# Kernel optimization log

Hardware: AMD Instinct MI355X
Metric: run time of the kernel (lower is better)

The kernel has to match this reference:

```python
import jax, jax.numpy as jnp
import numpy as np

B, L, D_MODEL, N_HEADS = 2, 2048, 2048, 16
HEAD_DIM = D_MODEL // N_HEADS
EPS = 1e-6
ROPE_THETA = 10000.0


def rms_norm(x, scale):
    # normalize over head_dim, learnable per-dim scale (QKNorm)
    var = jnp.mean(jnp.square(x), axis=-1, keepdims=True)
    return x * jax.lax.rsqrt(var + EPS) * scale


def rope(x, offset=0):
    # x: [B, H, T, D]; rotate-half rotary embedding over flattened positions
    T, D = x.shape[-2], x.shape[-1]
    half = D // 2
    inv_freq = 1.0 / (ROPE_THETA ** (jnp.arange(0, half, dtype=jnp.float32) / half))
    pos = jnp.arange(T, dtype=jnp.float32) + offset
    ang = pos[:, None] * inv_freq[None, :]            # [T, half]
    cos, sin = jnp.cos(ang), jnp.sin(ang)
    x1, x2 = x[..., :half], x[..., half:]
    return jnp.concatenate([x1 * cos - x2 * sin, x1 * sin + x2 * cos], axis=-1)


def setup_inputs() -> dict:
    key = jax.random.key(0)
    ks = jax.random.split(key, 7)
    s = 1.0 / np.sqrt(D_MODEL)
    x = jax.random.normal(ks[0], (B, L, D_MODEL), dtype=jnp.float32)
    w_qkv = jax.random.uniform(ks[1], (D_MODEL, 3 * D_MODEL), jnp.float32, -s, s)
    b_qkv = jax.random.uniform(ks[2], (3 * D_MODEL,), jnp.float32, -s, s)
    q_scale = jnp.ones((HEAD_DIM,), jnp.float32)
    k_scale = jnp.ones((HEAD_DIM,), jnp.float32)
    w_out = jax.random.uniform(ks[3], (D_MODEL, D_MODEL), jnp.float32, -s, s)
    b_out = jax.random.uniform(ks[4], (D_MODEL,), jnp.float32, -s, s)
    mask = jnp.tril(jnp.ones((L, L), dtype=bool))   # causal block mask pattern
    return {"x": x, "w_qkv": w_qkv, "b_qkv": b_qkv, "q_scale": q_scale,
            "k_scale": k_scale, "w_out": w_out, "b_out": b_out, "mask": mask}


def reference(x, w_qkv, b_qkv, q_scale, k_scale, w_out, b_out, mask):
    b, t, _ = x.shape
    qkv = x @ w_qkv + b_qkv                                   # [B, T, 3*D]
    qkv = qkv.reshape(b, t, 3, N_HEADS, HEAD_DIM)
    q, k, v = jnp.moveaxis(qkv, 2, 0)                          # each [B, T, H, D]
    q = jnp.transpose(q, (0, 2, 1, 3))                         # [B, H, T, D]
    k = jnp.transpose(k, (0, 2, 1, 3))
    v = jnp.transpose(v, (0, 2, 1, 3))
    q = rms_norm(q, q_scale)
    k = rms_norm(k, k_scale)
    q = rope(q, offset=0)
    k = rope(k, offset=0)
    scores = jnp.einsum('bhqd,bhkd->bhqk', q, k) / np.sqrt(HEAD_DIM)
    scores = jnp.where(mask[None, None, :, :], scores, jnp.float32(-1e30))
    attn = jax.nn.softmax(scores, axis=-1)
    out = jnp.einsum('bhqk,bhkd->bhqd', attn, v)               # [B, H, T, D]
    out = jnp.transpose(out, (0, 2, 1, 3)).reshape(b, t, D_MODEL)
    return out @ w_out + b_out
```

## Files before the change

kernel.cpp:

```cpp
#include <hip/hip_runtime.h>
#include <hip/hip_bf16.h>
#include <stdint.h>


typedef unsigned short ushort8 __attribute__((ext_vector_type(8)));
typedef short          bf16x8 __attribute__((ext_vector_type(8)));
typedef float          f32x4  __attribute__((ext_vector_type(4)));

#define B_   2
#define L_   2048
#define DM   2048
#define NH   16
#define HD   128
#define QKVW 6144

__device__ __forceinline__ uint16_t f2bf(float f){
  uint32_t u = __builtin_bit_cast(uint32_t, f);
  u += 0x7FFFu + ((u >> 16) & 1u);
  return (uint16_t)(u >> 16);
}
__device__ __forceinline__ float bf2f(uint16_t h){
  uint32_t u = ((uint32_t)h) << 16;
  return __builtin_bit_cast(float, u);
}

#define GLD16(gp, lp) __builtin_amdgcn_global_load_lds( \
  (const __attribute__((address_space(1))) void*)(gp),  \
  (__attribute__((address_space(3))) void*)(lp), 16, 0, 0)

__global__ __launch_bounds__(256) void rope_table(float* __restrict__ ct, float* __restrict__ st){
  int i = blockIdx.x * 256 + threadIdx.x;
  int t = i >> 6, d = i & 63;
  float invf = powf(10000.f, -(float)d * (1.f/64.f));
  float s, c;
  sincosf((float)t * invf, &s, &c);
  ct[i] = c; st[i] = s;
}

__global__ __launch_bounds__(256) void cvt_f32_bf16(const float* __restrict__ x,
                                                    uint16_t* __restrict__ o, int n8){
  int i = blockIdx.x * 256 + threadIdx.x;
  if (i < n8){
    const float4* xv = (const float4*)x;
    float4 a = xv[(size_t)i*2], b = xv[(size_t)i*2+1];
    ushort8 v;
    v[0]=f2bf(a.x); v[1]=f2bf(a.y); v[2]=f2bf(a.z); v[3]=f2bf(a.w);
    v[4]=f2bf(b.x); v[5]=f2bf(b.y); v[6]=f2bf(b.z); v[7]=f2bf(b.w);
    *(ushort8*)(o + (size_t)i*8) = v;
  }
}

__global__ __launch_bounds__(256) void transpose_w(const float* __restrict__ W,
                                                   uint16_t* __restrict__ Wt, int R, int C){
  __shared__ float T[64][65];
  const int rb = blockIdx.x, cb = blockIdx.y;
  const int tid = threadIdx.x;
#pragma unroll
  for (int i=0;i<4;i++){
    int rr = i*16 + (tid >> 4);
    int cc = (tid & 15) * 4;
    float4 v = *(const float4*)(W + (size_t)(rb*64 + rr) * C + cb*64 + cc);
    T[rr][cc] = v.x; T[rr][cc+1] = v.y; T[rr][cc+2] = v.z; T[rr][cc+3] = v.w;
  }
  __syncthreads();
  const int oc = tid >> 2, rc = (tid & 3) * 16;
  ushort8 o0, o1;
#pragma unroll
  for (int j=0;j<8;j++){ o0[j] = f2bf(T[rc+j][oc]); o1[j] = f2bf(T[rc+8+j][oc]); }
  size_t ob = (size_t)(cb*64 + oc) * R + rb*64 + rc;
  *(ushort8*)(Wt + ob)     = o0;
  *(ushort8*)(Wt + ob + 8) = o1;
}

template<int MODE>
__global__ __launch_bounds__(512, 2) void gemm8p(
    const uint16_t* __restrict__ A, const uint16_t* __restrict__ Bt,
    const float* __restrict__ bias, void* __restrict__ Cv,
    int M, int N, int K, int nbn,
    const float* __restrict__ qs, const float* __restrict__ ks,
    const float* __restrict__ ct, const float* __restrict__ st)
{
  __shared__ uint16_t LA[3*16384];
  __shared__ uint16_t LB[3*8192];
  __shared__ float sums[4][2][64];
  const int nwg = (M >> 8) * nbn;
  const int q8  = nwg >> 3;
  const int id  = ((int)blockIdx.x & 7) * q8 + ((int)blockIdx.x >> 3);
  const int bm = id / nbn, bn = id % nbn;
  const int tid = threadIdx.x;
  const int lane = tid & 63, w = tid >> 6;
  const int wm = w & 3, wn = w >> 2;
  const int l15 = lane & 15, lh = lane >> 4;
  const int NT = K >> 6;

  const int qs3 = ((lane & 7) ^ ((lane >> 3) & 7)) * 8;
  const uint16_t* gA_ = A  + (size_t)((bm << 8) + (w << 5) + (lane >> 3)) * K + qs3;
  const uint16_t* gB_ = Bt + (size_t)((bn << 7) + (w << 4) + (lane >> 3)) * K + qs3;
  uint16_t* lA_ = LA + (w << 11);
  uint16_t* lB_ = LB + (w << 10);

  const int sw0 = ((lh       ^ (l15 & 7)) << 3);
  const int sw1 = (((4 | lh) ^ (l15 & 7)) << 3);
  const int aoff = (((wm << 6) + l15) << 6);
  const int boff = (((wn << 5) + l15) << 6);
  const int bno[4] = {0, 1024, 4096, 5120};

  f32x4 acc[4][4];
#pragma unroll
  for (int i=0;i<4;i++)
#pragma unroll
    for (int j=0;j<4;j++) acc[i][j] = f32x4{0.f,0.f,0.f,0.f};

  auto STAGE_A = [&](int tt, int s, int i){
    GLD16(gA_ + (size_t)tt*64 + (size_t)(i*8)*K, lA_ + s*16384 + i*512);
  };
  auto STAGE_B = [&](int tt, int s, int i){
    GLD16(gB_ + (size_t)tt*64 + (size_t)(i*8)*K, lB_ + s*8192 + i*512);
  };

#pragma unroll
  for (int i=0;i<4;i++) STAGE_A(0, 0, i);
#pragma unroll
  for (int i=0;i<2;i++) STAGE_B(0, 0, i);
#pragma unroll
  for (int i=0;i<4;i++) STAGE_A(1, 1, i);
#pragma unroll
  for (int i=0;i<2;i++) STAGE_B(1, 1, i);
  asm volatile("s_waitcnt vmcnt(6)" ::: "memory");
  __builtin_amdgcn_s_barrier();

  int sl = 0, sl2 = 2;
  for (int t = 0; t < NT; ++t){
    const bool pf = (t + 2 < NT);
    const uint16_t* la = LA + sl*16384;
    const uint16_t* lb = LB + sl*8192;

    bf16x8 af0[4], bf0[4], af1[4], bf1[4];
#pragma unroll
    for (int mi=0;mi<4;mi++) af0[mi] = *(const bf16x8*)(la + aoff + mi*1024 + sw0);
#pragma unroll
    for (int ni=0;ni<4;ni++) bf0[ni] = *(const bf16x8*)(lb + boff + bno[ni] + sw0);
#pragma unroll
    for (int mi=0;mi<4;mi++) af1[mi] = *(const bf16x8*)(la + aoff + mi*1024 + sw1);
#pragma unroll
    for (int ni=0;ni<4;ni++) bf1[ni] = *(const bf16x8*)(lb + boff + bno[ni] + sw1);
    if (pf){
      STAGE_A(t+2, sl2, 0); STAGE_A(t+2, sl2, 1);
      STAGE_A(t+2, sl2, 2); STAGE_A(t+2, sl2, 3);
      STAGE_B(t+2, sl2, 0); STAGE_B(t+2, sl2, 1);
    }
    __builtin_amdgcn_s_setprio(1);
#pragma unroll
    for (int mi=0;mi<4;mi++)
#pragma unroll
      for (int ni=0;ni<4;ni++)
        acc[mi][ni] = __builtin_amdgcn_mfma_f32_16x16x32_bf16(af0[mi], bf0[ni], acc[mi][ni], 0, 0, 0);
#pragma unroll
    for (int mi=0;mi<4;mi++)
#pragma unroll
      for (int ni=0;ni<4;ni++)
        acc[mi][ni] = __builtin_amdgcn_mfma_f32_16x16x32_bf16(af1[mi], bf1[ni], acc[mi][ni], 0, 0, 0);
    __builtin_amdgcn_s_setprio(0);

    if (t < NT-2)       { asm volatile("s_waitcnt vmcnt(6)" ::: "memory"); }
    else if (t == NT-2) { asm volatile("s_waitcnt vmcnt(0)" ::: "memory"); }
    if (t < NT-1) __builtin_amdgcn_s_barrier();
    sl  = (sl  == 2) ? 0 : sl  + 1;
    sl2 = (sl2 == 2) ? 0 : sl2 + 1;
  }

  const int cm = (bm << 8) + (wm << 6);
  const int cn = (bn << 7);
  int dc[4];
#pragma unroll
  for (int ni=0;ni<4;ni++) dc[ni] = (wn<<5) + ((ni>>1)<<6) + ((ni&1)<<4) + l15;
  float bs[4];
#pragma unroll
  for (int ni=0;ni<4;ni++) bs[ni] = bias[cn + dc[ni]];

  if (MODE == 0){
#pragma unroll
    for (int mi=0;mi<4;mi++)
#pragma unroll
      for (int r=0;r<4;r++){
        int rowg = cm + mi*16 + lh*4 + r;
#pragma unroll
        for (int ni=0;ni<4;ni++)
          ((float*)Cv)[(size_t)rowg * N + cn + dc[ni]] = acc[mi][ni][r] + bs[ni];
      }
  } else {
    uint16_t* Cb = (uint16_t*)Cv;
    const int part = bn >> 4;
    if (part == 2){
#pragma unroll
      for (int mi=0;mi<4;mi++)
#pragma unroll
        for (int r=0;r<4;r++){
          int rowg = cm + mi*16 + lh*4 + r;
#pragma unroll
          for (int ni=0;ni<4;ni++)
            Cb[(size_t)rowg * N + cn + dc[ni]] = f2bf(acc[mi][ni][r] + bs[ni]);
        }
    } else {
      const float* scp = part ? ks : qs;
      float scv[4];
#pragma unroll
      for (int ni=0;ni<4;ni++) scv[ni] = scp[dc[ni]];
      float ssum[4][4];
#pragma unroll
      for (int mi=0;mi<4;mi++)
#pragma unroll
        for (int r=0;r<4;r++){
          float s = 0.f;
#pragma unroll
          for (int ni=0;ni<4;ni++){
            float v = acc[mi][ni][r] + bs[ni];
            acc[mi][ni][r] = v;
            s += v*v;
          }
          s += __shfl_xor(s, 1); s += __shfl_xor(s, 2);
          s += __shfl_xor(s, 4); s += __shfl_xor(s, 8);
          ssum[mi][r] = s;
        }
      if (l15 == 0){
#pragma unroll
        for (int mi=0;mi<4;mi++)
#pragma unroll
          for (int r=0;r<4;r++) sums[wm][wn][mi*16 + lh*4 + r] = ssum[mi][r];
      }
      __syncthreads();
      const int dd0 = (wn<<5) + l15, dd1 = dd0 + 16;
#pragma unroll
      for (int mi=0;mi<4;mi++){
#pragma unroll
        for (int r=0;r<4;r++){
          int rid = mi*16 + lh*4 + r;
          float tot = ssum[mi][r] + sums[wm][wn^1][rid];
          float iv = rsqrtf(tot * 0.0078125f + 1e-6f);
          int rowg = cm + rid;
          int t = rowg & (L_-1);
          float y0 = acc[mi][0][r] * iv * scv[0];
          float y1 = acc[mi][1][r] * iv * scv[1];
          float y2 = acc[mi][2][r] * iv * scv[2];
          float y3 = acc[mi][3][r] * iv * scv[3];
          float c0 = ct[t*64 + dd0], s0 = st[t*64 + dd0];
          float c1 = ct[t*64 + dd1], s1 = st[t*64 + dd1];
          size_t rb_ = (size_t)rowg * N + cn;
          Cb[rb_ + dc[0]] = f2bf(y0*c0 - y2*s0);
          Cb[rb_ + dc[1]] = f2bf(y1*c1 - y3*s1);
          Cb[rb_ + dc[2]] = f2bf(y0*s0 + y2*c0);
          Cb[rb_ + dc[3]] = f2bf(y1*s1 + y3*c1);
        }
      }
    }
  }
}

__global__ __launch_bounds__(256) void transpose_v(const uint16_t* __restrict__ qkv,
                                                   uint16_t* __restrict__ vt){
  __shared__ uint16_t T[64][136];
  const int tb = blockIdx.x, bh = blockIdx.y;
  const int b = bh >> 4, h = bh & 15;
  const int tid = threadIdx.x;
#pragma unroll
  for (int i=0;i<4;i++){
    int g = i*256 + tid, tt = g >> 4, c = g & 15;
    *(ushort8*)(&T[tt][c*8]) =
      *(const ushort8*)(qkv + ((size_t)b*L_ + tb*64 + tt)*QKVW + 2*DM + h*HD + c*8);
  }
  __syncthreads();
  const int d = tid >> 1, th = tid & 1;
#pragma unroll
  for (int i=0;i<4;i++){
    ushort8 o;
#pragma unroll
    for (int j=0;j<8;j++) o[j] = T[th*32 + i*8 + j][d];
    *(ushort8*)(vt + ((size_t)bh*HD + d)*L_ + tb*64 + th*32 + i*8) = o;
  }
}

__global__ __launch_bounds__(256) void flash_attn(
    const uint16_t* __restrict__ qkv, const uint16_t* __restrict__ vt,
    uint16_t* __restrict__ ao)
{
  const int qp = blockIdx.x;
  const int bh = blockIdx.y;
  const int b = bh >> 4, h = bh & 15;
  const int tid = threadIdx.x;
  const int lane = tid & 63, w = tid >> 6;
  const int l15 = lane & 15, lh = lane >> 4;

  __shared__ uint16_t Ks[64][136];
  __shared__ uint16_t Vs[128][72];
  __shared__ uint16_t Ps[4][16][72];

  const float SCL = 0.12751744f;

  for (int sel = 0; sel < 2; sel++){
    const int qb = sel ? (31 - qp) : qp;

    const size_t qrow = (size_t)b * L_ + qb*64 + w*16 + l15;
    const uint16_t* qp_ = qkv + qrow * QKVW + h * HD;
    bf16x8 qf[4];
#pragma unroll
    for (int c = 0; c < 4; c++) qf[c] = *(const bf16x8*)(qp_ + c*32 + lh*8);

    float m_s = -3.0e38f, l_s = 0.f;
    f32x4 oacc[8];
#pragma unroll
    for (int nt = 0; nt < 8; nt++) oacc[nt] = f32x4{0.f,0.f,0.f,0.f};

    const int ntile = qb + 1;
    ushort8 rk[4], rv[4];

#pragma unroll
    for (int i = 0; i < 4; i++){
      int g = i*256 + tid, row = g >> 4, c = g & 15;
      rk[i] = *(const ushort8*)(qkv + ((size_t)b*L_ + row)*QKVW + DM + h*HD + c*8);
    }
#pragma unroll
    for (int i = 0; i < 4; i++){
      int g = i*256 + tid, d = g >> 3, c = g & 7;
      rv[i] = *(const ushort8*)(vt + ((size_t)bh*HD + d)*L_ + c*8);
    }

    for (int kt = 0; kt < ntile; kt++){
      __syncthreads();
#pragma unroll
      for (int i = 0; i < 4; i++){ int g = i*256+tid; *(ushort8*)(&Ks[g>>4][(g&15)*8]) = rk[i]; }
#pragma unroll
      for (int i = 0; i < 4; i++){ int g = i*256+tid; *(ushort8*)(&Vs[g>>3][(g&7)*8]) = rv[i]; }
      __syncthreads();

      if (kt + 1 < ntile){
        const int k2 = (kt + 1) * 64;
#pragma unroll
        for (int i = 0; i < 4; i++){
          int g = i*256 + tid, row = g >> 4, c = g & 15;
          rk[i] = *(const ushort8*)(qkv + ((size_t)b*L_ + k2 + row)*QKVW + DM + h*HD + c*8);
        }
#pragma unroll
        for (int i = 0; i < 4; i++){
          int g = i*256 + tid, d = g >> 3, c = g & 7;
          rv[i] = *(const ushort8*)(vt + ((size_t)bh*HD + d)*L_ + k2 + c*8);
        }
      }

      f32x4 s[4];
#pragma unroll
      for (int nt = 0; nt < 4; nt++) s[nt] = f32x4{0.f,0.f,0.f,0.f};
      __builtin_amdgcn_s_setprio(1);
#pragma unroll
      for (int c = 0; c < 4; c++){
#pragma unroll
        for (int nt = 0; nt < 4; nt++){
          bf16x8 kf = *(const bf16x8*)(&Ks[nt*16 + l15][c*32 + lh*8]);
          s[nt] = __builtin_amdgcn_mfma_f32_16x16x32_bf16(kf, qf[c], s[nt], 0, 0, 0);
        }
      }
      __builtin_amdgcn_s_setprio(0);

      const bool diag = (kt == qb);
      const int qg = w*16 + l15;
      const int kb = lh*4;
#pragma unroll
      for (int nt = 0; nt < 4; nt++){
#pragma unroll
        for (int r = 0; r < 4; r++){
          float v = s[nt][r] * SCL;
          if (diag && (nt*16 + kb + r > qg)) v = -1.0e30f;
          s[nt][r] = v;
        }
      }
      float pm = s[0][0];
#pragma unroll
      for (int nt = 0; nt < 4; nt++)
#pragma unroll
        for (int r = 0; r < 4; r++) pm = fmaxf(pm, s[nt][r]);
      pm = fmaxf(pm, __shfl_xor(pm, 16));
      pm = fmaxf(pm, __shfl_xor(pm, 32));
      if (!__all(pm - m_s <= 8.0f)){
        float mn = fmaxf(m_s, pm);
        float alpha = exp2f(m_s - mn);
        m_s = mn; l_s *= alpha;
        float ar[4];
#pragma unroll
        for (int r = 0; r < 4; r++) ar[r] = __shfl(alpha, lh*4 + r);
#pragma unroll
        for (int nt = 0; nt < 8; nt++)
#pragma unroll
          for (int r = 0; r < 4; r++) oacc[nt][r] *= ar[r];
      }
      float rs = 0.f;
#pragma unroll
      for (int nt = 0; nt < 4; nt++){
        float p0 = exp2f(s[nt][0] - m_s);
        float p1 = exp2f(s[nt][1] - m_s);
        float p2 = exp2f(s[nt][2] - m_s);
        float p3 = exp2f(s[nt][3] - m_s);
        rs += (p0 + p1) + (p2 + p3);
        uint2 pk;
        pk.x = (uint32_t)f2bf(p0) | ((uint32_t)f2bf(p1) << 16);
        pk.y = (uint32_t)f2bf(p2) | ((uint32_t)f2bf(p3) << 16);
        *(uint2*)(&Ps[w][l15][nt*16 + kb]) = pk;
      }
      rs += __shfl_xor(rs, 16);
      rs += __shfl_xor(rs, 32);
      l_s += rs;

      asm volatile("s_waitcnt lgkmcnt(0)" ::: "memory");
      __builtin_amdgcn_s_setprio(1);
#pragma unroll
      for (int kc = 0; kc < 2; kc++){
        bf16x8 pf = *(const bf16x8*)(&Ps[w][l15][kc*32 + lh*8]);
#pragma unroll
        for (int nt = 0; nt < 8; nt++){
          bf16x8 vf = *(const bf16x8*)(&Vs[nt*16 + l15][kc*32 + lh*8]);
          oacc[nt] = __builtin_amdgcn_mfma_f32_16x16x32_bf16(pf, vf, oacc[nt], 0, 0, 0);
        }
      }
      __builtin_amdgcn_s_setprio(0);
    }
    float invl[4];
#pragma unroll
    for (int r = 0; r < 4; r++) invl[r] = 1.f / __shfl(l_s, lh*4 + r);
#pragma unroll
    for (int nt = 0; nt < 8; nt++){
#pragma unroll
      for (int r = 0; r < 4; r++){
        float v = oacc[nt][r] * invl[r];
        size_t row = (size_t)b*L_ + qb*64 + w*16 + lh*4 + r;
        ao[row * DM + h*HD + nt*16 + l15] = f2bf(v);
      }
    }
  }
}

extern "C" void kernel_launch(void* const* d_in, const int* in_sizes, int n_in,
                              void* d_out, int out_size, void* d_ws, size_t ws_size,
                              hipStream_t stream)
{
  (void)in_sizes; (void)n_in; (void)out_size; (void)ws_size;
  const float* x       = (const float*)d_in[0];
  const float* w_qkv   = (const float*)d_in[1];
  const float* b_qkv   = (const float*)d_in[2];
  const float* q_scale = (const float*)d_in[3];
  const float* k_scale = (const float*)d_in[4];
  const float* w_out   = (const float*)d_in[5];
  const float* b_out   = (const float*)d_in[6];
  float* out = (float*)d_out;

  char* ws = (char*)d_ws;
  uint16_t* qkv   = (uint16_t*)(ws);
  uint16_t* reg1  = (uint16_t*)(ws + 50331648);
  uint16_t* reg2  = (uint16_t*)(ws + 50331648 + 16777216);
  uint16_t* woutT = (uint16_t*)(ws + 50331648 + 16777216 + 25165824);
  float*    ct    = (float*)(ws + 100663296);
  float*    st    = ct + 131072;

  uint16_t* xb    = reg1;
  uint16_t* ao    = reg1;
  uint16_t* wqkvT = reg2;
  uint16_t* vt    = reg2;

  rope_table  <<<512, 256, 0, stream>>>(ct, st);
  cvt_f32_bf16<<<4096, 256, 0, stream>>>(x, xb, 1048576);
  transpose_w <<<dim3(32, 96), 256, 0, stream>>>(w_qkv, wqkvT, 2048, 6144);
  transpose_w <<<dim3(32, 32), 256, 0, stream>>>(w_out, woutT, 2048, 2048);
  gemm8p<1>   <<<768, 512, 0, stream>>>(xb, wqkvT, b_qkv, qkv, 4096, 6144, 2048, 48,
                                        q_scale, k_scale, ct, st);
  transpose_v <<<dim3(32, 32), 256, 0, stream>>>(qkv, vt);
  flash_attn  <<<dim3(16, 32), 256, 0, stream>>>(qkv, vt, ao);
  gemm8p<0>   <<<256, 512, 0, stream>>>(ao, woutT, b_out, out, 4096, 2048, 2048, 16,
                                        nullptr, nullptr, nullptr, nullptr);
}
```

Before: 273.2 us.

## Double-buffer K/V tiles in LDS with XOR swizzle, one barrier per tile

The flash attention loop now keeps two LDS buffers for K and V. The next tile is written into the spare buffer after the QK MFMAs, and global loads are issued two tiles ahead, so each iteration needs one barrier instead of two. The padded LDS rows are replaced by an XOR swizzle of 16-byte chunks on K, V and P to avoid bank conflicts without padding. This doubles LDS use for K/V, which may lower occupancy, and makes the indexing more complex.

```diff
diff --git a/kernel.cpp b/kernel.cpp
--- a/kernel.cpp
+++ b/kernel.cpp
@@ -289,10 +289,11 @@
   const int tid = threadIdx.x;
   const int lane = tid & 63, w = tid >> 6;
   const int l15 = lane & 15, lh = lane >> 4;
-
-  __shared__ uint16_t Ks[64][136];
-  __shared__ uint16_t Vs[128][72];
-  __shared__ uint16_t Ps[4][16][72];
+  const int e3 = l15 & 7;
+
+  __shared__ uint16_t Ks[2][64][128];
+  __shared__ uint16_t Vs[2][128][64];
+  __shared__ uint16_t Ps[4][16][64];
 
   const float SCL = 0.12751744f;
 
@@ -313,6 +314,7 @@
     const int ntile = qb + 1;
     ushort8 rk[4], rv[4];
 
+    __syncthreads();
 #pragma unroll
     for (int i = 0; i < 4; i++){
       int g = i*256 + tid, row = g >> 4, c = g & 15;
@@ -323,42 +325,72 @@
       int g = i*256 + tid, d = g >> 3, c = g & 7;
       rv[i] = *(const ushort8*)(vt + ((size_t)bh*HD + d)*L_ + c*8);
     }
+#pragma unroll
+    for (int i = 0; i < 4; i++){
+      int g = i*256 + tid, row = g >> 4, c = g & 15;
+      *(ushort8*)(&Ks[0][row][(c ^ (row & 7))*8]) = rk[i];
+    }
+#pragma unroll
+    for (int i = 0; i < 4; i++){
+      int g = i*256 + tid, d = g >> 3, c = g & 7;
+      *(ushort8*)(&Vs[0][d][(c ^ (d & 7))*8]) = rv[i];
+    }
+    if (ntile > 1){
+#pragma unroll
+      for (int i = 0; i < 4; i++){
+        int g = i*256 + tid, row = g >> 4, c = g & 15;
+        rk[i] = *(const ushort8*)(qkv + ((size_t)b*L_ + 64 + row)*QKVW + DM + h*HD + c*8);
+      }
+#pragma unroll
+      for (int i = 0; i < 4; i++){
+        int g = i*256 + tid, d = g >> 3, c = g & 7;
+        rv[i] = *(const ushort8*)(vt + ((size_t)bh*HD + d)*L_ + 64 + c*8);
+      }
+    }
+    __syncthreads();
 
     for (int kt = 0; kt < ntile; kt++){
-      __syncthreads();
-#pragma unroll
-      for (int i = 0; i < 4; i++){ int g = i*256+tid; *(ushort8*)(&Ks[g>>4][(g&15)*8]) = rk[i]; }
-#pragma unroll
-      for (int i = 0; i < 4; i++){ int g = i*256+tid; *(ushort8*)(&Vs[g>>3][(g&7)*8]) = rv[i]; }
-      __syncthreads();
-
-      if (kt + 1 < ntile){
-        const int k2 = (kt + 1) * 64;
-#pragma unroll
-        for (int i = 0; i < 4; i++){
-          int g = i*256 + tid, row = g >> 4, c = g & 15;
-          rk[i] = *(const ushort8*)(qkv + ((size_t)b*L_ + k2 + row)*QKVW + DM + h*HD + c*8);
-        }
-#pragma unroll
-        for (int i = 0; i < 4; i++){
-          int g = i*256 + tid, d = g >> 3, c = g & 7;
-          rv[i] = *(const ushort8*)(vt + ((size_t)bh*HD + d)*L_ + k2 + c*8);
-        }
-      }
+      const int c = kt & 1;
 
       f32x4 s[4];
 #pragma unroll
       for (int nt = 0; nt < 4; nt++) s[nt] = f32x4{0.f,0.f,0.f,0.f};
       __builtin_amdgcn_s_setprio(1);
 #pragma unroll
-      for (int c = 0; c < 4; c++){
+      for (int cc = 0; cc < 4; cc++){
 #pragma unroll
         for (int nt = 0; nt < 4; nt++){
-          bf16x8 kf = *(const bf16x8*)(&Ks[nt*16 + l15][c*32 + lh*8]);
-          s[nt] = __builtin_amdgcn_mfma_f32_16x16x32_bf16(kf, qf[c], s[nt], 0, 0, 0);
+          bf16x8 kf = *(const bf16x8*)(&Ks[c][nt*16 + l15][(((cc<<2)|lh) ^ e3)*8]);
+          s[nt] = __builtin_amdgcn_mfma_f32_16x16x32_bf16(kf, qf[cc], s[nt], 0, 0, 0);
         }
       }
       __builtin_amdgcn_s_setprio(0);
+
+      if (kt + 1 < ntile){
+#pragma unroll
+        for (int i = 0; i < 4; i++){
+          int g = i*256 + tid, row = g >> 4, cc = g & 15;
+          *(ushort8*)(&Ks[c^1][row][(cc ^ (row & 7))*8]) = rk[i];
+        }
+#pragma unroll
+        for (int i = 0; i < 4; i++){
+          int g = i*256 + tid, d = g >> 3, cc = g & 7;
+          *(ushort8*)(&Vs[c^1][d][(cc ^ (d & 7))*8]) = rv[i];
+        }
+      }
+      if (kt + 2 < ntile){
+        const int k2 = (kt + 2) * 64;
+#pragma unroll
+        for (int i = 0; i < 4; i++){
+          int g = i*256 + tid, row = g >> 4, cc = g & 15;
+          rk[i] = *(const ushort8*)(qkv + ((size_t)b*L_ + k2 + row)*QKVW + DM + h*HD + cc*8);
+        }
+#pragma unroll
+        for (int i = 0; i < 4; i++){
+          int g = i*256 + tid, d = g >> 3, cc = g & 7;
+          rv[i] = *(const ushort8*)(vt + ((size_t)bh*HD + d)*L_ + k2 + cc*8);
+        }
+      }
 
       const bool diag = (kt == qb);
       const int qg = w*16 + l15;
@@ -402,7 +434,8 @@
         uint2 pk;
         pk.x = (uint32_t)f2bf(p0) | ((uint32_t)f2bf(p1) << 16);
         pk.y = (uint32_t)f2bf(p2) | ((uint32_t)f2bf(p3) << 16);
-        *(uint2*)(&Ps[w][l15][nt*16 + kb]) = pk;
+        int ch = ((nt<<1) | (lh>>1)) ^ e3;
+        *(uint2*)(&Ps[w][l15][ch*8 + (lh&1)*4]) = pk;
       }
       rs += __shfl_xor(rs, 16);
       rs += __shfl_xor(rs, 32);
@@ -412,14 +445,16 @@
       __builtin_amdgcn_s_setprio(1);
 #pragma unroll
       for (int kc = 0; kc < 2; kc++){
-        bf16x8 pf = *(const bf16x8*)(&Ps[w][l15][kc*32 + lh*8]);
+        bf16x8 pf = *(const bf16x8*)(&Ps[w][l15][(((kc<<2)|lh) ^ e3)*8]);
 #pragma unroll
         for (int nt = 0; nt < 8; nt++){
-          bf16x8 vf = *(const bf16x8*)(&Vs[nt*16 + l15][kc*32 + lh*8]);
+          bf16x8 vf = *(const bf16x8*)(&Vs[c][nt*16 + l15][(((kc<<2)|lh) ^ e3)*8]);
           oacc[nt] = __builtin_amdgcn_mfma_f32_16x16x32_bf16(pf, vf, oacc[nt], 0, 0, 0);
         }
       }
       __builtin_amdgcn_s_setprio(0);
+
+      if (kt + 1 < ntile) __syncthreads();
     }
     float invl[4];
 #pragma unroll
```

After: 298.3 us. +9.2%, slower.
